# Performance work log

Hardware: AMD Instinct MI355X
Metric: run time of the kernel (lower is better)

The kernel has to match this reference:

```python
import jax, jax.numpy as jnp
import numpy as np

BRANCH, VOCAB, FFN, BATCH = 8, 256, 1024, 16384
LN_EPS = 1e-5


def setup_inputs() -> dict:
    key = jax.random.key(0)
    ks = jax.random.split(key, 7)
    x = jax.random.normal(ks[0], (BATCH, BRANCH, VOCAB), dtype=jnp.float32)
    U1 = 0.01 * jax.random.normal(ks[1], (BRANCH, VOCAB, FFN), dtype=jnp.float32)
    b1 = 0.01 * jax.random.normal(ks[2], (BRANCH, FFN), dtype=jnp.float32)
    U2 = 0.01 * jax.random.normal(ks[3], (BRANCH, FFN, VOCAB), dtype=jnp.float32)
    b2 = 0.01 * jax.random.normal(ks[4], (BRANCH, VOCAB), dtype=jnp.float32)
    ln_w = jnp.ones((VOCAB,), dtype=jnp.float32)
    ln_b = jnp.zeros((VOCAB,), dtype=jnp.float32)
    return {"x": x, "U1": U1, "b1": b1, "U2": U2, "b2": b2, "ln_w": ln_w, "ln_b": ln_b}


def _layernorm(h, w, b):
    mu = jnp.mean(h, axis=-1, keepdims=True)
    var = jnp.var(h, axis=-1, keepdims=True)
    return (h - mu) * jax.lax.rsqrt(var + LN_EPS) * w + b


def reference(x, U1, b1, U2, b2, ln_w, ln_b):
    # x: (B, N, D); branch-wise batched GEMMs via einsum (avoids explicit permutes)
    skip = x
    h = jnp.einsum('bnd,nde->bne', x, U1) + b1        # (B, N, FFN)
    h = jax.nn.gelu(h, approximate=False)
    h = jnp.einsum('bne,ned->bnd', h, U2) + b2        # (B, N, VOCAB)
    h = _layernorm(h, ln_w, ln_b)
    h = jax.nn.gelu(h, approximate=False)
    out = skip + h
    return out.reshape(BATCH, 1, BRANCH * VOCAB)
```

## Files before the change

kernel.cpp:

```cpp
#include <hip/hip_runtime.h>
#include <hip/hip_bf16.h>

#define NBR   8
#define DV    256
#define FF    1024
#define RT    64
#define NCH   32
#define NROWS 16384

#define L_B1 0
#define L_HS 32768
#define LDS_BYTES 36864

using bf16x8 = __attribute__((ext_vector_type(8))) short;
using f32x4  = __attribute__((ext_vector_type(4))) float;

__device__ __forceinline__ unsigned short f2bf(float f) {
    unsigned int u = __builtin_bit_cast(unsigned int, f);
    unsigned int r = (u + 0x7fffu + ((u >> 16) & 1u)) >> 16;
    return (unsigned short)r;
}
__device__ __forceinline__ float gelu_fast(float x) {
    float x2 = x * x;
    float z  = x * fmaf(x2, -0.1029434959f, -2.3022078770f);
    float e  = __builtin_amdgcn_exp2f(z);
    return x * __builtin_amdgcn_rcpf(1.0f + e);
}

#define GLL(gsrc, ldst) __builtin_amdgcn_global_load_lds((const unsigned int*)(gsrc), (unsigned int*)(ldst), 16, 0, 0)
#define MFMA16 __builtin_amdgcn_mfma_f32_16x16x32_bf16

__global__ void prep_weights(const float* __restrict__ U1, const float* __restrict__ U2,
                             unsigned short* __restrict__ w1img, unsigned short* __restrict__ w2img)
{
    const int b = blockIdx.x;
    const int n = b >> 5, cch = b & 31;
    const int tid = threadIdx.x;
    char* img1 = (char*)w1img + ((size_t)b << 14);
    char* img2 = (char*)w2img + ((size_t)b << 14);
    const float* U1n = U1 + (size_t)n * DV * FF;
    const float* U2n = U2 + (size_t)n * FF * DV;
    #pragma unroll
    for (int e = 0; e < 4; ++e) {
        int p = tid + e * 256;
        int kkg = p >> 5, nn = p & 31;
        bf16x8 h;
        #pragma unroll
        for (int j = 0; j < 8; ++j)
            h[j] = (short)f2bf(U1n[(size_t)(kkg * 8 + j) * FF + cch * 32 + nn]);
        *(bf16x8*)(img1 + kkg * 512 + nn * 16) = h;
    }
    #pragma unroll
    for (int e = 0; e < 4; ++e) {
        int p = tid + e * 256;
        int cfg = p >> 6, l = p & 63;
        bf16x8 h;
        #pragma unroll
        for (int j = 0; j < 8; ++j)
            h[j] = (short)f2bf(U2n[(size_t)(cch * 32 + (l >> 4) * 8 + j) * DV + cfg * 16 + (l & 15)]);
        *(bf16x8*)(img2 + (p << 4)) = h;
    }
}

__global__ __launch_bounds__(512, 4)
void belayer_main(const float* __restrict__ x,
                  const unsigned short* __restrict__ w1img,
                  const unsigned short* __restrict__ w2img,
                  const float* __restrict__ b1g, const float* __restrict__ b2g,
                  const float* __restrict__ lnw, const float* __restrict__ lnb,
                  float* __restrict__ out)
{
    __shared__ __align__(16) char LDS[LDS_BYTES];
    const int tid  = threadIdx.x;
    const int lane = tid & 63;
    const int wave = tid >> 6;
    const int q = lane >> 4, c = lane & 15;
    const int n    = blockIdx.x & 7;
    const int tile = blockIdx.x >> 3;
    const int row0 = tile * RT;
    const int rowg   = wave >> 1;
    const int colsel = wave & 1;
    const int rowg2  = wave >> 2;
    const int colg2  = wave & 3;

    const char* g1base = (const char*)w1img + ((size_t)(n * NCH) << 14) + (wave << 11) + lane * 16;
    const char* g2img  = (const char*)w2img + ((size_t)(n * NCH) << 14) + (colg2 << 12) + lane * 16;
    char* l1base = LDS + L_B1 + (wave << 11);

#define STAGE1(T) do { const char* g_ = g1base + ((size_t)(T) << 14); \
        char* l_ = l1base + (((T) & 1) << 14); GLL(g_, l_); GLL(g_ + 1024, l_ + 1024); } while (0)

    STAGE1(0);

    bf16x8 A[8];
    {
        const float* src = x + (((size_t)(row0 + rowg * 16 + c)) * NBR + n) * DV + q * 8;
        #pragma unroll
        for (int ks = 0; ks < 8; ++ks) {
            f32x4 v0 = *(const f32x4*)(src + ks * 32);
            f32x4 v1 = *(const f32x4*)(src + ks * 32 + 4);
            bf16x8 h;
            h[0] = (short)f2bf(v0[0]); h[1] = (short)f2bf(v0[1]);
            h[2] = (short)f2bf(v0[2]); h[3] = (short)f2bf(v0[3]);
            h[4] = (short)f2bf(v1[0]); h[5] = (short)f2bf(v1[1]);
            h[6] = (short)f2bf(v1[2]); h[7] = (short)f2bf(v1[3]);
            A[ks] = h;
        }
    }

    const unsigned aB1 = (unsigned)(q * 512 + (colsel * 16 + c) * 16);
    unsigned aW[4];
    #pragma unroll
    for (int r = 0; r < 4; ++r)
        aW[r] = (unsigned)(((colsel * 2 + (c >> 3)) * 64 + rowg * 16 + q * 4 + r) * 16 + (c & 7) * 2);
    const unsigned aH = (unsigned)((q * 64 + rowg2 * 32 + c) * 16);

    f32x4 acc2[2][4];
    #pragma unroll
    for (int i = 0; i < 2; ++i)
        #pragma unroll
        for (int j = 0; j < 4; ++j) acc2[i][j] = (f32x4){0.f, 0.f, 0.f, 0.f};

    __syncthreads();

    for (int t = 0; t < NCH; ++t) {
        const unsigned h1 = L_B1 + ((unsigned)(t & 1) << 14);

        bf16x8 B2f[4];
        #pragma unroll
        for (int cf = 0; cf < 4; ++cf)
            B2f[cf] = *(const bf16x8*)(g2img + ((size_t)t << 14) + (cf << 10));
        if (t + 1 < NCH) STAGE1(t + 1);
        float b1v = b1g[n * FF + t * 32 + colsel * 16 + c];
        f32x4 acc1 = (f32x4){0.f, 0.f, 0.f, 0.f};
        #pragma unroll
        for (int ks = 0; ks < 8; ++ks) {
            bf16x8 b = *(const bf16x8*)(LDS + h1 + aB1 + ks * 2048);
            acc1 = MFMA16(A[ks], b, acc1, 0, 0, 0);
        }
        #pragma unroll
        for (int r = 0; r < 4; ++r) {
            float g = gelu_fast(acc1[r] + b1v);
            *(unsigned short*)(LDS + L_HS + aW[r]) = f2bf(g);
        }
        __syncthreads();

        bf16x8 a0 = *(const bf16x8*)(LDS + L_HS + aH);
        bf16x8 a1 = *(const bf16x8*)(LDS + L_HS + aH + 256);
        #pragma unroll
        for (int cf = 0; cf < 4; ++cf) {
            acc2[0][cf] = MFMA16(a0, B2f[cf], acc2[0][cf], 0, 0, 0);
            acc2[1][cf] = MFMA16(a1, B2f[cf], acc2[1][cf], 0, 0, 0);
        }
        __syncthreads();
    }

    float b2v[4];
    #pragma unroll
    for (int cf = 0; cf < 4; ++cf) b2v[cf] = b2g[n * DV + colg2 * 64 + cf * 16 + c];

    float sA[2][4], sQ[2][4];
    #pragma unroll
    for (int rf = 0; rf < 2; ++rf)
        #pragma unroll
        for (int r = 0; r < 4; ++r) { sA[rf][r] = 0.f; sQ[rf][r] = 0.f; }
    #pragma unroll
    for (int rf = 0; rf < 2; ++rf)
        #pragma unroll
        for (int cf = 0; cf < 4; ++cf)
            #pragma unroll
            for (int r = 0; r < 4; ++r) {
                float v = acc2[rf][cf][r] + b2v[cf];
                acc2[rf][cf][r] = v;
                sA[rf][r] += v;
                sQ[rf][r] += v * v;
            }
    #pragma unroll
    for (int m = 1; m < 16; m <<= 1)
        #pragma unroll
        for (int rf = 0; rf < 2; ++rf)
            #pragma unroll
            for (int r = 0; r < 4; ++r) {
                sA[rf][r] += __shfl_xor(sA[rf][r], m, 64);
                sQ[rf][r] += __shfl_xor(sQ[rf][r], m, 64);
            }
    float* Lred = (float*)(LDS + L_HS);
    if (c == 0) {
        #pragma unroll
        for (int rf = 0; rf < 2; ++rf)
            #pragma unroll
            for (int r = 0; r < 4; ++r) {
                int row = rowg2 * 32 + rf * 16 + q * 4 + r;
                Lred[row * 4 + colg2]       = sA[rf][r];
                Lred[256 + row * 4 + colg2] = sQ[rf][r];
            }
    }
    __syncthreads();
    float mu[2][4], rs[2][4];
    #pragma unroll
    for (int rf = 0; rf < 2; ++rf)
        #pragma unroll
        for (int r = 0; r < 4; ++r) {
            int row = rowg2 * 32 + rf * 16 + q * 4 + r;
            f32x4 sv = *(const f32x4*)(Lred + row * 4);
            f32x4 qv = *(const f32x4*)(Lred + 256 + row * 4);
            float ssum = sv[0] + sv[1] + sv[2] + sv[3];
            float qsum = qv[0] + qv[1] + qv[2] + qv[3];
            float m_ = ssum * (1.0f / 256.0f);
            float var = qsum * (1.0f / 256.0f) - m_ * m_;
            mu[rf][r] = m_;
            rs[rf][r] = rsqrtf(var + 1e-5f);
        }
    #pragma unroll
    for (int cf = 0; cf < 4; ++cf) {
        int col = colg2 * 64 + cf * 16 + c;
        float lw = lnw[col];
        float lb = lnb[col];
        #pragma unroll
        for (int rf = 0; rf < 2; ++rf)
            #pragma unroll
            for (int r = 0; r < 4; ++r) {
                int row = rowg2 * 32 + rf * 16 + q * 4 + r;
                float v = (acc2[rf][cf][r] - mu[rf][r]) * rs[rf][r] * lw + lb;
                float g = gelu_fast(v);
                size_t oi = ((size_t)(row0 + row) * NBR + n) * DV + col;
                out[oi] = x[oi] + g;
            }
    }
#undef STAGE1
}

extern "C" void kernel_launch(void* const* d_in, const int* in_sizes, int n_in,
                              void* d_out, int out_size, void* d_ws, size_t ws_size,
                              hipStream_t stream) {
    const float* x   = (const float*)d_in[0];
    const float* U1  = (const float*)d_in[1];
    const float* b1  = (const float*)d_in[2];
    const float* U2  = (const float*)d_in[3];
    const float* b2  = (const float*)d_in[4];
    const float* lnw = (const float*)d_in[5];
    const float* lnb = (const float*)d_in[6];
    float* out = (float*)d_out;

    unsigned short* w1img = (unsigned short*)d_ws;
    unsigned short* w2img = w1img + (size_t)4 * 1024 * 1024 / 2;

    prep_weights<<<dim3(256), dim3(256), 0, stream>>>(U1, U2, w1img, w2img);
    belayer_main<<<dim3((NROWS / RT) * NBR), dim3(512), 0, stream>>>(x, w1img, w2img, b1, b2, lnw, lnb, out);
}
```

Measured before the change: 236.1 us.

## Double FFN chunk width and software-pipeline GEMM1 with GEMM2 across iterations

```diff
diff --git a/kernel.cpp b/kernel.cpp
--- a/kernel.cpp
+++ b/kernel.cpp
@@ -5,12 +5,12 @@
 #define DV    256
 #define FF    1024
 #define RT    64
-#define NCH   32
+#define NCH   16
 #define NROWS 16384
 
 #define L_B1 0
-#define L_HS 32768
-#define LDS_BYTES 36864
+#define L_HS 65536
+#define LDS_BYTES 81920
 
 using bf16x8 = __attribute__((ext_vector_type(8))) short;
 using f32x4  = __attribute__((ext_vector_type(4))) float;
@@ -34,31 +34,32 @@
                              unsigned short* __restrict__ w1img, unsigned short* __restrict__ w2img)
 {
     const int b = blockIdx.x;
-    const int n = b >> 5, cch = b & 31;
+    const int n = b >> 4, cch = b & 15;
     const int tid = threadIdx.x;
-    char* img1 = (char*)w1img + ((size_t)b << 14);
-    char* img2 = (char*)w2img + ((size_t)b << 14);
+    char* img1 = (char*)w1img + ((size_t)b << 15);
+    char* img2 = (char*)w2img + ((size_t)b << 15);
     const float* U1n = U1 + (size_t)n * DV * FF;
     const float* U2n = U2 + (size_t)n * FF * DV;
     #pragma unroll
-    for (int e = 0; e < 4; ++e) {
+    for (int e = 0; e < 8; ++e) {
         int p = tid + e * 256;
-        int kkg = p >> 5, nn = p & 31;
+        int kkg = p >> 6, nn = p & 63;
         bf16x8 h;
         #pragma unroll
         for (int j = 0; j < 8; ++j)
-            h[j] = (short)f2bf(U1n[(size_t)(kkg * 8 + j) * FF + cch * 32 + nn]);
-        *(bf16x8*)(img1 + kkg * 512 + nn * 16) = h;
-    }
-    #pragma unroll
-    for (int e = 0; e < 4; ++e) {
+            h[j] = (short)f2bf(U1n[(size_t)(kkg * 8 + j) * FF + cch * 64 + nn]);
+        *(bf16x8*)(img1 + ((size_t)p << 4)) = h;
+    }
+    #pragma unroll
+    for (int e = 0; e < 8; ++e) {
         int p = tid + e * 256;
-        int cfg = p >> 6, l = p & 63;
+        int f = p >> 6, l = p & 63;
+        int ks = f >> 4, cfg = f & 15;
         bf16x8 h;
         #pragma unroll
         for (int j = 0; j < 8; ++j)
-            h[j] = (short)f2bf(U2n[(size_t)(cch * 32 + (l >> 4) * 8 + j) * DV + cfg * 16 + (l & 15)]);
-        *(bf16x8*)(img2 + (p << 4)) = h;
+            h[j] = (short)f2bf(U2n[(size_t)(cch * 64 + ks * 32 + (l >> 4) * 8 + j) * DV + cfg * 16 + (l & 15)]);
+        *(bf16x8*)(img2 + ((size_t)p << 4)) = h;
     }
 }
 
@@ -83,12 +84,13 @@
     const int rowg2  = wave >> 2;
     const int colg2  = wave & 3;
 
-    const char* g1base = (const char*)w1img + ((size_t)(n * NCH) << 14) + (wave << 11) + lane * 16;
-    const char* g2img  = (const char*)w2img + ((size_t)(n * NCH) << 14) + (colg2 << 12) + lane * 16;
-    char* l1base = LDS + L_B1 + (wave << 11);
-
-#define STAGE1(T) do { const char* g_ = g1base + ((size_t)(T) << 14); \
-        char* l_ = l1base + (((T) & 1) << 14); GLL(g_, l_); GLL(g_ + 1024, l_ + 1024); } while (0)
+    const char* g1base = (const char*)w1img + ((size_t)(n * NCH) << 15) + (wave << 12) + lane * 16;
+    const char* g2base = (const char*)w2img + ((size_t)(n * NCH) << 15) + ((unsigned)(colg2 * 4) << 10) + lane * 16;
+    char* l1base = LDS + L_B1 + (wave << 12);
+
+#define STAGE1(T) do { const char* g_ = g1base + ((size_t)(T) << 15); \
+        char* l_ = l1base + (((T) & 1) << 15); \
+        GLL(g_, l_); GLL(g_ + 1024, l_ + 1024); GLL(g_ + 2048, l_ + 2048); GLL(g_ + 3072, l_ + 3072); } while (0)
 
     STAGE1(0);
 
@@ -108,11 +110,11 @@
         }
     }
 
-    const unsigned aB1 = (unsigned)(q * 512 + (colsel * 16 + c) * 16);
-    unsigned aW[4];
-    #pragma unroll
-    for (int r = 0; r < 4; ++r)
-        aW[r] = (unsigned)(((colsel * 2 + (c >> 3)) * 64 + rowg * 16 + q * 4 + r) * 16 + (c & 7) * 2);
+    const unsigned aB1 = (unsigned)((colsel * 32 + c) * 16);
+    unsigned aWb[2];
+    #pragma unroll
+    for (int cf = 0; cf < 2; ++cf)
+        aWb[cf] = (unsigned)(((colsel * 4 + cf * 2 + (c >> 3)) * 64 + rowg * 16 + q * 4) * 16 + (c & 7) * 2);
     const unsigned aH = (unsigned)((q * 64 + rowg2 * 32 + c) * 16);
 
     f32x4 acc2[2][4];
@@ -123,34 +125,56 @@
 
     __syncthreads();
 
-    for (int t = 0; t < NCH; ++t) {
-        const unsigned h1 = L_B1 + ((unsigned)(t & 1) << 14);
-
-        bf16x8 B2f[4];
-        #pragma unroll
-        for (int cf = 0; cf < 4; ++cf)
-            B2f[cf] = *(const bf16x8*)(g2img + ((size_t)t << 14) + (cf << 10));
+    for (int t = 0; t <= NCH; ++t) {
+        bf16x8 B2f[2][4];
+        if (t >= 1) {
+            #pragma unroll
+            for (int ks = 0; ks < 2; ++ks)
+                #pragma unroll
+                for (int cf = 0; cf < 4; ++cf)
+                    B2f[ks][cf] = *(const bf16x8*)(g2base + ((size_t)(t - 1) << 15) + (ks << 14) + (cf << 10));
+        }
         if (t + 1 < NCH) STAGE1(t + 1);
-        float b1v = b1g[n * FF + t * 32 + colsel * 16 + c];
-        f32x4 acc1 = (f32x4){0.f, 0.f, 0.f, 0.f};
-        #pragma unroll
-        for (int ks = 0; ks < 8; ++ks) {
-            bf16x8 b = *(const bf16x8*)(LDS + h1 + aB1 + ks * 2048);
-            acc1 = MFMA16(A[ks], b, acc1, 0, 0, 0);
-        }
-        #pragma unroll
-        for (int r = 0; r < 4; ++r) {
-            float g = gelu_fast(acc1[r] + b1v);
-            *(unsigned short*)(LDS + L_HS + aW[r]) = f2bf(g);
-        }
-        __syncthreads();
-
-        bf16x8 a0 = *(const bf16x8*)(LDS + L_HS + aH);
-        bf16x8 a1 = *(const bf16x8*)(LDS + L_HS + aH + 256);
-        #pragma unroll
-        for (int cf = 0; cf < 4; ++cf) {
-            acc2[0][cf] = MFMA16(a0, B2f[cf], acc2[0][cf], 0, 0, 0);
-            acc2[1][cf] = MFMA16(a1, B2f[cf], acc2[1][cf], 0, 0, 0);
+
+        if (t < NCH) {
+            float b1v0 = b1g[n * FF + t * 64 + colsel * 32 + c];
+            float b1v1 = b1g[n * FF + t * 64 + colsel * 32 + 16 + c];
+            const unsigned h1 = L_B1 + ((unsigned)(t & 1) << 15);
+            f32x4 acc1[2];
+            acc1[0] = (f32x4){0.f, 0.f, 0.f, 0.f};
+            acc1[1] = (f32x4){0.f, 0.f, 0.f, 0.f};
+            #pragma unroll
+            for (int ks = 0; ks < 8; ++ks) {
+                const unsigned base = h1 + (unsigned)(ks * 4 + q) * 1024 + aB1;
+                bf16x8 b0 = *(const bf16x8*)(LDS + base);
+                bf16x8 b1 = *(const bf16x8*)(LDS + base + 256);
+                acc1[0] = MFMA16(A[ks], b0, acc1[0], 0, 0, 0);
+                acc1[1] = MFMA16(A[ks], b1, acc1[1], 0, 0, 0);
+            }
+            const unsigned hw = L_HS + ((unsigned)(t & 1) << 13);
+            #pragma unroll
+            for (int cf = 0; cf < 2; ++cf) {
+                float bv = cf ? b1v1 : b1v0;
+                #pragma unroll
+                for (int r = 0; r < 4; ++r) {
+                    float g = gelu_fast(acc1[cf][r] + bv);
+                    *(unsigned short*)(LDS + hw + aWb[cf] + r * 16) = f2bf(g);
+                }
+            }
+        }
+
+        if (t >= 1) {
+            const unsigned hp = L_HS + ((unsigned)((t - 1) & 1) << 13);
+            #pragma unroll
+            for (int ks = 0; ks < 2; ++ks) {
+                bf16x8 a0 = *(const bf16x8*)(LDS + hp + aH + ks * 4096);
+                bf16x8 a1 = *(const bf16x8*)(LDS + hp + aH + ks * 4096 + 256);
+                #pragma unroll
+                for (int cf = 0; cf < 4; ++cf) {
+                    acc2[0][cf] = MFMA16(a0, B2f[ks][cf], acc2[0][cf], 0, 0, 0);
+                    acc2[1][cf] = MFMA16(a1, B2f[ks][cf], acc2[1][cf], 0, 0, 0);
+                }
+            }
         }
         __syncthreads();
     }
@@ -245,6 +269,6 @@
     unsigned short* w1img = (unsigned short*)d_ws;
     unsigned short* w2img = w1img + (size_t)4 * 1024 * 1024 / 2;
 
-    prep_weights<<<dim3(256), dim3(256), 0, stream>>>(U1, U2, w1img, w2img);
+    prep_weights<<<dim3(128), dim3(256), 0, stream>>>(U1, U2, w1img, w2img);
     belayer_main<<<dim3((NROWS / RT) * NBR), dim3(512), 0, stream>>>(x, w1img, w2img, b1, b2, lnw, lnb, out);
 }
```

After: 244.3 us. +3.5%, slower.
